# Performance work log

Measured on AMD Instinct MI355X. Metric: run time of the kernel, lower is better.

Reference implementation:

```python
import jax, jax.numpy as jnp
import numpy as np

B, S, D = 16, 2048, 768
NORM = 1.0 / float(np.sqrt(D))


def setup_inputs() -> dict:
    key = jax.random.key(0)
    k1, k2, k3, k4, k5 = jax.random.split(key, 5)
    b_in = jax.random.normal(k1, (B, S, D), dtype=jnp.float32)
    mask = jax.random.randint(k2, (B, S), 0, 2, dtype=jnp.int64)
    # row 0 must be unmasked: the module returns attention[:, 0, :], and a fully
    # masked query row softmaxes all -inf -> NaN (same quirk as the torch source).
    mask = mask.at[:, 0].set(1)
    Wq = jax.random.normal(k3, (D, D), dtype=jnp.float32) * 0.02
    Wk = jax.random.normal(k4, (D, D), dtype=jnp.float32) * 0.02
    Wv = jax.random.normal(k5, (D, D), dtype=jnp.float32) * 0.02
    return {"b_in": b_in, "mask": mask, "Wq": Wq, "Wk": Wk, "Wv": Wv}


def reference(b_in, mask, Wq, Wk, Wv):
    # nn.Linear(bias=False): y = x @ W.T  (W is [out, in])
    q = jnp.einsum("bsd,ed->bse", b_in, Wq)
    k = jnp.einsum("bsd,ed->bse", b_in, Wk)
    v = jnp.einsum("bsd,ed->bse", b_in, Wv)
    # full [B, S, S] score matrix, as in the original bmm
    scores = jnp.einsum("bqd,bkd->bqk", q, k) * NORM
    # mask.unsqueeze(2): [B, S, 1] broadcasts over the KEY axis -> masks whole query rows
    scores = jnp.where(mask[:, :, None] == 0, -jnp.inf, scores)
    attn = jax.nn.softmax(scores, axis=-1)
    out = jnp.einsum("bqk,bkd->bqd", attn, v)
    return out[:, 0, :]
```

## Files before the change

### kernel.cpp

```cpp
#include <hip/hip_runtime.h>
#include <math.h>

#define BB 16
#define SS 2048
#define DD 768

#define NORM_SCALE 0.036084391824351615f

#define ECH 24
#define EPC (DD / ECH)

#define RPC 16
#define NCH (SS / RPC)

__global__ void rowdot_kernel(const float* __restrict__ src, size_t src_stride,
                              const float* __restrict__ W,
                              float* __restrict__ dst, float scale,
                              float* __restrict__ zero_buf) {
    int wid  = blockIdx.x * 4 + (threadIdx.x >> 6);
    int lane = threadIdx.x & 63;
    int b = wid / DD;
    int e = wid % DD;
    const float4* xr = (const float4*)(src + (size_t)b * src_stride);
    const float4* wr = (const float4*)(W + (size_t)e * DD);
    float acc = 0.f;
#pragma unroll
    for (int k = 0; k < 3; ++k) {
        float4 xv = xr[lane + k * 64];
        float4 wv = wr[lane + k * 64];
        acc += xv.x * wv.x + xv.y * wv.y + xv.z * wv.z + xv.w * wv.w;
    }
#pragma unroll
    for (int off = 32; off > 0; off >>= 1) acc += __shfl_down(acc, off);
    if (lane == 0) dst[wid] = acc * scale;
    if (zero_buf != nullptr && lane == 1) zero_buf[wid] = 0.f;
}

__global__ void kq_split_kernel(const float* __restrict__ q0,
                                const float* __restrict__ Wk,
                                float* __restrict__ kqs) {
    __shared__ float qs[EPC];
    int echunk = blockIdx.x;
    int b      = blockIdx.y;
    int t      = threadIdx.x;
    if (t < EPC) qs[t] = q0[b * DD + echunk * EPC + t];
    __syncthreads();
    const float4* Wk4 = (const float4*)(Wk + (size_t)(echunk * EPC) * DD);
    float4 acc = {0.f, 0.f, 0.f, 0.f};
#pragma unroll 4
    for (int e = 0; e < EPC; ++e) {
        float q = qs[e];
        float4 w = Wk4[e * (DD / 4) + t];
        acc.x += q * w.x;
        acc.y += q * w.y;
        acc.z += q * w.z;
        acc.w += q * w.w;
    }
    float* dst = kqs + b * DD + t * 4;
    atomicAdd(dst + 0, acc.x);
    atomicAdd(dst + 1, acc.y);
    atomicAdd(dst + 2, acc.z);
    atomicAdd(dst + 3, acc.w);
}

__global__ void __launch_bounds__(256) flash_kernel(
        const float* __restrict__ x,
        const float* __restrict__ kqs,
        float* __restrict__ m_part,
        float* __restrict__ l_part,
        float* __restrict__ o_part) {
    __shared__ float xs[RPC * DD];
    __shared__ float sc[RPC];
    __shared__ float p[RPC];
    __shared__ float mbc[1];
    int chunk = blockIdx.x;
    int b     = blockIdx.y;
    int tid   = threadIdx.x;
    int wave  = tid >> 6, lane = tid & 63;
    int s0    = chunk * RPC;

    const float* xg = x + ((size_t)b * SS + s0 + wave * 4) * DD;
    float*       xl = xs + wave * 4 * DD;
#pragma unroll
    for (int k = 0; k < 12; ++k) {
        __builtin_amdgcn_global_load_lds(
            (const __attribute__((address_space(1))) unsigned int*)(xg + k * 256 + lane * 4),
            (__attribute__((address_space(3))) unsigned int*)(xl + k * 256),
            16, 0, 0);
    }

    const float4* kr = (const float4*)(kqs + b * DD);
    float4 kf0 = kr[lane];
    float4 kf1 = kr[lane + 64];
    float4 kf2 = kr[lane + 128];

    __syncthreads();

#pragma unroll
    for (int j = 0; j < 4; ++j) {
        int r = wave * 4 + j;
        const float4* xsr = (const float4*)(xs + r * DD);
        float4 x0 = xsr[lane];
        float4 x1 = xsr[lane + 64];
        float4 x2 = xsr[lane + 128];
        float acc = x0.x * kf0.x + x0.y * kf0.y + x0.z * kf0.z + x0.w * kf0.w
                  + x1.x * kf1.x + x1.y * kf1.y + x1.z * kf1.z + x1.w * kf1.w
                  + x2.x * kf2.x + x2.y * kf2.y + x2.z * kf2.z + x2.w * kf2.w;
#pragma unroll
        for (int off = 32; off > 0; off >>= 1) acc += __shfl_down(acc, off);
        if (lane == 0) sc[r] = acc;
    }
    __syncthreads();

    if (tid == 0) {
        float m = sc[0];
#pragma unroll
        for (int r = 1; r < RPC; ++r) m = fmaxf(m, sc[r]);
        mbc[0] = m;
    }
    __syncthreads();
    if (tid < RPC) p[tid] = expf(sc[tid] - mbc[0]);
    __syncthreads();

    float a0 = 0.f, a1 = 0.f, a2 = 0.f;
#pragma unroll
    for (int r = 0; r < RPC; ++r) {
        float pr = p[r];
        a0 += pr * xs[r * DD + tid];
        a1 += pr * xs[r * DD + tid + 256];
        a2 += pr * xs[r * DD + tid + 512];
    }
    int pidx = b * NCH + chunk;
    float* op = o_part + (size_t)pidx * DD;
    op[tid]       = a0;
    op[tid + 256] = a1;
    op[tid + 512] = a2;
    if (tid == 0) {
        float l = 0.f;
#pragma unroll
        for (int r = 0; r < RPC; ++r) l += p[r];
        m_part[pidx] = mbc[0];
        l_part[pidx] = l;
    }
}

__global__ void combine_kernel(const float* __restrict__ m_part,
                               const float* __restrict__ l_part,
                               const float* __restrict__ o_part,
                               float* __restrict__ c) {
    __shared__ float w[NCH];
    __shared__ float bc[2];
    int b   = blockIdx.x;
    int seg = blockIdx.y;
    int tid = threadIdx.x;

    if (tid < NCH) w[tid] = m_part[b * NCH + tid];
    __syncthreads();
    if (tid == 0) {
        float M = w[0];
        for (int i = 1; i < NCH; ++i) M = fmaxf(M, w[i]);
        bc[0] = M;
    }
    __syncthreads();
    float M = bc[0];
    if (tid < NCH) w[tid] = expf(w[tid] - M);
    __syncthreads();
    if (tid == 0) {
        float l = 0.f;
        for (int i = 0; i < NCH; ++i) l += w[i] * l_part[b * NCH + i];
        bc[1] = 1.f / l;
    }
    __syncthreads();
    float inv = bc[1];

    int col = seg * 256 + tid;
    const float* op = o_part + (size_t)b * NCH * DD + col;
    float a = 0.f;
#pragma unroll 8
    for (int cc = 0; cc < NCH; ++cc) a += w[cc] * op[(size_t)cc * DD];
    c[b * DD + col] = a * inv;
}

extern "C" void kernel_launch(void* const* d_in, const int* in_sizes, int n_in,
                              void* d_out, int out_size, void* d_ws, size_t ws_size,
                              hipStream_t stream) {
    const float* b_in = (const float*)d_in[0];
    const float* Wq = (const float*)d_in[2];
    const float* Wk = (const float*)d_in[3];
    const float* Wv = (const float*)d_in[4];
    float* out = (float*)d_out;

    float* ws     = (float*)d_ws;
    float* q0     = ws;
    float* kqs    = q0 + BB * DD;
    float* m_part = kqs + BB * DD;
    float* l_part = m_part + BB * NCH;
    float* o_part = l_part + BB * NCH;
    float* c      = o_part + (size_t)BB * NCH * DD;

    rowdot_kernel<<<BB * DD / 4, 256, 0, stream>>>(b_in, (size_t)SS * DD, Wq,
                                                   q0, NORM_SCALE, kqs);
    kq_split_kernel<<<dim3(ECH, BB), 192, 0, stream>>>(q0, Wk, kqs);
    flash_kernel<<<dim3(NCH, BB), 256, 0, stream>>>(b_in, kqs,
                                                    m_part, l_part, o_part);
    combine_kernel<<<dim3(BB, 3), 256, 0, stream>>>(m_part, l_part, o_part, c);
    rowdot_kernel<<<BB * DD / 4, 256, 0, stream>>>(c, (size_t)DD, Wv, out,
                                                   1.f, nullptr);
}
```

Baseline: 185.5 us.

## Keep flash chunk rows in registers and use wave-parallel reductions in combine

The flash kernel now loads each wave's four x rows straight into registers instead of staging all 16 rows in LDS through global_load_lds. It computes the weighted sum per wave from registers and reduces the four wave partials through a small LDS buffer. Every thread computes the chunk max redundantly, which removes two barriers and the serial single-thread steps. The combine kernel swaps its serial max and sum loops for wave shuffle reductions. LDS use per block drops sharply, which may raise occupancy, at the cost of about 48 extra VGPRs per thread.

After: 182.2 us. About the same (-1.7%).

```diff
diff --git a/kernel.cpp b/kernel.cpp
--- a/kernel.cpp
+++ b/kernel.cpp
@@ -69,78 +69,77 @@
         float* __restrict__ m_part,
         float* __restrict__ l_part,
         float* __restrict__ o_part) {
-    __shared__ float xs[RPC * DD];
+    __shared__ float4 osh[4 * 192];
     __shared__ float sc[RPC];
-    __shared__ float p[RPC];
-    __shared__ float mbc[1];
+    __shared__ float wsum[4];
     int chunk = blockIdx.x;
     int b     = blockIdx.y;
     int tid   = threadIdx.x;
     int wave  = tid >> 6, lane = tid & 63;
     int s0    = chunk * RPC;
 
-    const float* xg = x + ((size_t)b * SS + s0 + wave * 4) * DD;
-    float*       xl = xs + wave * 4 * DD;
-#pragma unroll
-    for (int k = 0; k < 12; ++k) {
-        __builtin_amdgcn_global_load_lds(
-            (const __attribute__((address_space(1))) unsigned int*)(xg + k * 256 + lane * 4),
-            (__attribute__((address_space(3))) unsigned int*)(xl + k * 256),
-            16, 0, 0);
-    }
+    const float4* xr = (const float4*)(x + ((size_t)b * SS + s0 + wave * 4) * DD);
+    float4 xv[12];
+#pragma unroll
+    for (int j = 0; j < 4; ++j)
+#pragma unroll
+        for (int k = 0; k < 3; ++k)
+            xv[j * 3 + k] = xr[j * (DD / 4) + k * 64 + lane];
 
     const float4* kr = (const float4*)(kqs + b * DD);
-    float4 kf0 = kr[lane];
-    float4 kf1 = kr[lane + 64];
-    float4 kf2 = kr[lane + 128];
-
-    __syncthreads();
+    float4 kf[3];
+#pragma unroll
+    for (int k = 0; k < 3; ++k) kf[k] = kr[k * 64 + lane];
 
 #pragma unroll
     for (int j = 0; j < 4; ++j) {
-        int r = wave * 4 + j;
-        const float4* xsr = (const float4*)(xs + r * DD);
-        float4 x0 = xsr[lane];
-        float4 x1 = xsr[lane + 64];
-        float4 x2 = xsr[lane + 128];
-        float acc = x0.x * kf0.x + x0.y * kf0.y + x0.z * kf0.z + x0.w * kf0.w
-                  + x1.x * kf1.x + x1.y * kf1.y + x1.z * kf1.z + x1.w * kf1.w
-                  + x2.x * kf2.x + x2.y * kf2.y + x2.z * kf2.z + x2.w * kf2.w;
+        float acc = 0.f;
+#pragma unroll
+        for (int k = 0; k < 3; ++k) {
+            float4 xx = xv[j * 3 + k];
+            acc += xx.x * kf[k].x + xx.y * kf[k].y
+                 + xx.z * kf[k].z + xx.w * kf[k].w;
+        }
 #pragma unroll
         for (int off = 32; off > 0; off >>= 1) acc += __shfl_down(acc, off);
-        if (lane == 0) sc[r] = acc;
-    }
-    __syncthreads();
-
+        if (lane == 0) sc[wave * 4 + j] = acc;
+    }
+    __syncthreads();
+
+    float m = sc[0];
+#pragma unroll
+    for (int r = 1; r < RPC; ++r) m = fmaxf(m, sc[r]);
+
+    float pl = (lane < 4) ? expf(sc[wave * 4 + lane] - m) : 0.f;
+    float p0 = __shfl(pl, 0), p1 = __shfl(pl, 1);
+    float p2 = __shfl(pl, 2), p3 = __shfl(pl, 3);
+    if (lane == 0) wsum[wave] = p0 + p1 + p2 + p3;
+
+#pragma unroll
+    for (int k = 0; k < 3; ++k) {
+        float4 a;
+        a.x = p0 * xv[k].x + p1 * xv[3 + k].x + p2 * xv[6 + k].x + p3 * xv[9 + k].x;
+        a.y = p0 * xv[k].y + p1 * xv[3 + k].y + p2 * xv[6 + k].y + p3 * xv[9 + k].y;
+        a.z = p0 * xv[k].z + p1 * xv[3 + k].z + p2 * xv[6 + k].z + p3 * xv[9 + k].z;
+        a.w = p0 * xv[k].w + p1 * xv[3 + k].w + p2 * xv[6 + k].w + p3 * xv[9 + k].w;
+        osh[wave * 192 + k * 64 + lane] = a;
+    }
+    __syncthreads();
+
+    int pidx = b * NCH + chunk;
+    if (tid < 192) {
+        float4 s0v = osh[tid], s1 = osh[192 + tid];
+        float4 s2 = osh[384 + tid], s3 = osh[576 + tid];
+        float4 s;
+        s.x = s0v.x + s1.x + s2.x + s3.x;
+        s.y = s0v.y + s1.y + s2.y + s3.y;
+        s.z = s0v.z + s1.z + s2.z + s3.z;
+        s.w = s0v.w + s1.w + s2.w + s3.w;
+        ((float4*)(o_part + (size_t)pidx * DD))[tid] = s;
+    }
     if (tid == 0) {
-        float m = sc[0];
-#pragma unroll
-        for (int r = 1; r < RPC; ++r) m = fmaxf(m, sc[r]);
-        mbc[0] = m;
-    }
-    __syncthreads();
-    if (tid < RPC) p[tid] = expf(sc[tid] - mbc[0]);
-    __syncthreads();
-
-    float a0 = 0.f, a1 = 0.f, a2 = 0.f;
-#pragma unroll
-    for (int r = 0; r < RPC; ++r) {
-        float pr = p[r];
-        a0 += pr * xs[r * DD + tid];
-        a1 += pr * xs[r * DD + tid + 256];
-        a2 += pr * xs[r * DD + tid + 512];
-    }
-    int pidx = b * NCH + chunk;
-    float* op = o_part + (size_t)pidx * DD;
-    op[tid]       = a0;
-    op[tid + 256] = a1;
-    op[tid + 512] = a2;
-    if (tid == 0) {
-        float l = 0.f;
-#pragma unroll
-        for (int r = 0; r < RPC; ++r) l += p[r];
-        m_part[pidx] = mbc[0];
-        l_part[pidx] = l;
+        m_part[pidx] = m;
+        l_part[pidx] = wsum[0] + wsum[1] + wsum[2] + wsum[3];
     }
 }
 
@@ -154,21 +153,22 @@
     int seg = blockIdx.y;
     int tid = threadIdx.x;
 
-    if (tid < NCH) w[tid] = m_part[b * NCH + tid];
-    __syncthreads();
-    if (tid == 0) {
-        float M = w[0];
-        for (int i = 1; i < NCH; ++i) M = fmaxf(M, w[i]);
-        bc[0] = M;
+    if (tid < 64) {
+        float m = fmaxf(m_part[b * NCH + tid], m_part[b * NCH + tid + 64]);
+#pragma unroll
+        for (int off = 32; off > 0; off >>= 1) m = fmaxf(m, __shfl_down(m, off));
+        if (tid == 0) bc[0] = m;
     }
     __syncthreads();
     float M = bc[0];
-    if (tid < NCH) w[tid] = expf(w[tid] - M);
-    __syncthreads();
-    if (tid == 0) {
-        float l = 0.f;
-        for (int i = 0; i < NCH; ++i) l += w[i] * l_part[b * NCH + i];
-        bc[1] = 1.f / l;
+    if (tid < NCH) w[tid] = expf(m_part[b * NCH + tid] - M);
+    __syncthreads();
+    if (tid < 64) {
+        float s = w[tid] * l_part[b * NCH + tid]
+                + w[tid + 64] * l_part[b * NCH + tid + 64];
+#pragma unroll
+        for (int off = 32; off > 0; off >>= 1) s += __shfl_down(s, off);
+        if (tid == 0) bc[1] = 1.f / s;
     }
     __syncthreads();
     float inv = bc[1];
```
